# Performance work log

Measured on AMD Instinct MI355X. Metric: run time of the kernel, lower is better.

## Reference

```python
import jax, jax.numpy as jnp
import numpy as np

B, D, H = 65536, 3, 256  # collocation batch, coord dim, hidden width


def setup_inputs() -> dict:
    key = jax.random.key(0)
    ks = jax.random.split(key, 8)

    def init(k, shape, fan_in):
        return jax.random.normal(k, shape, dtype=jnp.float32) * np.float32(1.0 / np.sqrt(fan_in))

    return {
        "x": jax.random.uniform(ks[0], (B, D), dtype=jnp.float32, minval=0.1, maxval=1.0),
        "W0": init(ks[1], (D, H), D), "b0": jnp.zeros((H,), jnp.float32),
        "W1": init(ks[2], (H, H), H), "b1": jnp.zeros((H,), jnp.float32),
        "W2": init(ks[3], (H, H), H), "b2": jnp.zeros((H,), jnp.float32),
        "W3": init(ks[4], (H, H), H), "b3": jnp.zeros((H,), jnp.float32),
        "Wout": init(ks[5], (H, 1), H), "bout": jnp.zeros((1,), jnp.float32),
    }


def reference(x, W0, b0, W1, b1, W2, b2, W3, b3, Wout, bout):
    # Scalar PINN network u(xi), xi: [D]
    def u_fn(xi):
        h = jnp.tanh(xi @ W0 + b0)
        h = jnp.tanh(h @ W1 + b1)
        h = jnp.tanh(h @ W2 + b2)
        h = jnp.tanh(h @ W3 + b3)
        return (h @ Wout + bout)[0]

    u = jax.vmap(u_fn)(x)                               # [B]
    # batch_gradient: du/dx_i for every coordinate axis (Cartesian: no adjustment)
    grads = jax.vmap(jax.grad(u_fn))(x)                 # [B, D]
    # batch_hessian diagonal: d^2u/dx_i^2 via forward-over-reverse
    hess_fn = jax.jacfwd(jax.grad(u_fn))                # [D, D] per sample
    hess_diag = jax.vmap(lambda xi: jnp.diagonal(hess_fn(xi)))(x)  # [B, D]
    # pack (u, grad, hessian-diagonal) as the PDE-residual ingredients
    return jnp.concatenate([u[:, None], grads, hess_diag], axis=1)  # [B, 1+D+D]
```

## Files before the change

kernel.cpp:

```cpp
#include <hip/hip_runtime.h>
#include <hip/hip_fp16.h>

#define HDIM 256
#define MS 16
#define PAD 8
#define LDAK (HDIM + PAD)

typedef _Float16 half8 __attribute__((ext_vector_type(8)));
typedef _Float16 half4 __attribute__((ext_vector_type(4)));
typedef float f32x4 __attribute__((ext_vector_type(4)));

__device__ __forceinline__ float fast_tanh(float x) {
    float e = __expf(2.0f * x);
    return 1.0f - 2.0f * __builtin_amdgcn_rcpf(e + 1.0f);
}

__global__ __launch_bounds__(256) void pack_weights(const float* __restrict__ W1,
                                                    const float* __restrict__ W2,
                                                    const float* __restrict__ W3,
                                                    _Float16* __restrict__ out) {
    int tid = blockIdx.x * blockDim.x + threadIdx.x;
    int l = tid >> 16;
    int idx = tid & 65535;
    int k = idx >> 8;
    int n = idx & 255;
    const float* W = (l == 0) ? W1 : (l == 1) ? W2 : W3;
    out[l * 65536 + (((k >> 3) << 8) + n) * 8 + (k & 7)] = (_Float16)W[idx];
}

__global__ __launch_bounds__(256, 2)
void pinn_fused(const float* __restrict__ x,
                const float* __restrict__ W0,
                const float* __restrict__ b0,
                const float* __restrict__ b1,
                const float* __restrict__ b2,
                const float* __restrict__ b3,
                const float* __restrict__ Wout,
                const float* __restrict__ bout,
                const _Float16* __restrict__ Wp,
                float* __restrict__ out) {
    __shared__ __align__(16) _Float16 Abuf[7 * MS][LDAK];
    __shared__ float xs[MS * 3];

    const int tid  = threadIdx.x;
    const int lane = tid & 63;
    const int wid  = tid >> 6;
    const int qd   = lane >> 4;
    const int n15  = lane & 15;
    const int base = blockIdx.x * MS;

    if (tid < MS * 3) xs[tid] = x[base * 3 + tid];
    __syncthreads();

    {
        const int m = tid & 15;
        const int n0base = (tid >> 4) * 16;
        const float x0 = xs[m * 3 + 0], x1 = xs[m * 3 + 1], x2 = xs[m * 3 + 2];
        #pragma unroll
        for (int ch = 0; ch < 4; ++ch) {
            const int n0 = n0base + ch * 4;
            f32x4 w0 = *(const f32x4*)(W0 + 0 * HDIM + n0);
            f32x4 w1 = *(const f32x4*)(W0 + 1 * HDIM + n0);
            f32x4 w2 = *(const f32x4*)(W0 + 2 * HDIM + n0);
            f32x4 bv = *(const f32x4*)(b0 + n0);
            half4 h[7];
            #pragma unroll
            for (int r = 0; r < 4; ++r) {
                float z  = x0 * w0[r] + x1 * w1[r] + x2 * w2[r] + bv[r];
                float tv = fast_tanh(z);
                float dd = 1.f - tv * tv;
                float c2 = -2.f * tv * dd;
                h[0][r] = (_Float16)tv;
                h[1][r] = (_Float16)(dd * w0[r]);
                h[2][r] = (_Float16)(dd * w1[r]);
                h[3][r] = (_Float16)(dd * w2[r]);
                h[4][r] = (_Float16)(c2 * w0[r] * w0[r]);
                h[5][r] = (_Float16)(c2 * w1[r] * w1[r]);
                h[6][r] = (_Float16)(c2 * w2[r] * w2[r]);
            }
            #pragma unroll
            for (int c = 0; c < 7; ++c)
                *(half4*)&Abuf[c * MS + m][n0] = h[c];
        }
    }
    __syncthreads();

    #pragma unroll
    for (int l = 0; l < 3; ++l) {
        const _Float16* W = Wp + l * 65536;
        const float* bb = (l == 0) ? b1 : (l == 1) ? b2 : b3;

        f32x4 acc[7][4];
        #pragma unroll
        for (int c = 0; c < 7; ++c)
            #pragma unroll
            for (int t = 0; t < 4; ++t) acc[c][t] = (f32x4){0.f, 0.f, 0.f, 0.f};

        #pragma unroll
        for (int s = 0; s < 8; ++s) {
            half8 wf[4];
            #pragma unroll
            for (int t = 0; t < 4; ++t) {
                const int n = wid * 64 + t * 16 + n15;
                wf[t] = *(const half8*)(W + ((s * 4 + qd) * 256 + n) * 8);
            }
            #pragma unroll
            for (int c = 0; c < 7; ++c) {
                half8 af = *(const half8*)&Abuf[c * MS + n15][s * 32 + qd * 8];
                #pragma unroll
                for (int t = 0; t < 4; ++t)
                    acc[c][t] = __builtin_amdgcn_mfma_f32_16x16x32_f16(wf[t], af, acc[c][t], 0, 0, 0);
            }
        }
        __syncthreads();

        #pragma unroll
        for (int t = 0; t < 4; ++t) {
            const int ncol = wid * 64 + t * 16 + qd * 4;
            f32x4 bv = *(const f32x4*)(bb + ncol);
            half4 h[7];
            #pragma unroll
            for (int r = 0; r < 4; ++r) {
                float zv = acc[0][t][r] + bv[r];
                float tv = fast_tanh(zv);
                float dd = 1.f - tv * tv;
                float c2 = -2.f * tv * dd;
                h[0][r] = (_Float16)tv;
                #pragma unroll
                for (int i = 0; i < 3; ++i) {
                    float zg = acc[1 + i][t][r];
                    float zs = acc[4 + i][t][r];
                    h[1 + i][r] = (_Float16)(dd * zg);
                    h[4 + i][r] = (_Float16)(dd * zs + c2 * zg * zg);
                }
            }
            #pragma unroll
            for (int c = 0; c < 7; ++c)
                *(half4*)&Abuf[c * MS + n15][ncol] = h[c];
        }
        __syncthreads();
    }

    if (tid < 7 * MS * 2) {
        const int row = tid >> 1;
        const int h   = tid & 1;
        const _Float16* rp = &Abuf[row][h * 128];
        const float* wp = Wout + h * 128;
        float accv = 0.f;
        #pragma unroll 4
        for (int k = 0; k < 128; k += 8) {
            half8 av = *(const half8*)&rp[k];
            #pragma unroll
            for (int j = 0; j < 8; ++j) accv += (float)av[j] * wp[k + j];
        }
        accv += __shfl_xor(accv, 1, 64);
        if (h == 0) {
            const int c = row >> 4;
            const int m = row & 15;
            if (c == 0) accv += bout[0];
            out[(base + m) * 7 + c] = accv;
        }
    }
}

extern "C" void kernel_launch(void* const* d_in, const int* in_sizes, int n_in,
                              void* d_out, int out_size, void* d_ws, size_t ws_size,
                              hipStream_t stream) {
    const float* xp   = (const float*)d_in[0];
    const float* W0   = (const float*)d_in[1];
    const float* b0   = (const float*)d_in[2];
    const float* W1   = (const float*)d_in[3];
    const float* b1   = (const float*)d_in[4];
    const float* W2   = (const float*)d_in[5];
    const float* b2   = (const float*)d_in[6];
    const float* W3   = (const float*)d_in[7];
    const float* b3   = (const float*)d_in[8];
    const float* Wout = (const float*)d_in[9];
    const float* bout = (const float*)d_in[10];
    _Float16* Wp = (_Float16*)d_ws;

    pack_weights<<<768, 256, 0, stream>>>(W1, W2, W3, Wp);
    pinn_fused<<<65536 / MS, 256, 0, stream>>>(xp, W0, b0, b1, b2, b3, Wout, bout, Wp,
                                               (float*)d_out);
}
```

Baseline: 267.8 us.

## Use 512-thread blocks with XOR-swizzled LDS and vectorized weight packing

```diff
diff --git a/kernel.cpp b/kernel.cpp
--- a/kernel.cpp
+++ b/kernel.cpp
@@ -3,8 +3,6 @@
 
 #define HDIM 256
 #define MS 16
-#define PAD 8
-#define LDAK (HDIM + PAD)
 
 typedef _Float16 half8 __attribute__((ext_vector_type(8)));
 typedef _Float16 half4 __attribute__((ext_vector_type(4)));
@@ -15,20 +13,27 @@
     return 1.0f - 2.0f * __builtin_amdgcn_rcpf(e + 1.0f);
 }
 
+__device__ __forceinline__ int swz(int row, int col) {
+    return (col & 0xC7) | (((((col >> 3) ^ row)) & 7) << 3);
+}
+
 __global__ __launch_bounds__(256) void pack_weights(const float* __restrict__ W1,
                                                     const float* __restrict__ W2,
                                                     const float* __restrict__ W3,
                                                     _Float16* __restrict__ out) {
-    int tid = blockIdx.x * blockDim.x + threadIdx.x;
-    int l = tid >> 16;
-    int idx = tid & 65535;
-    int k = idx >> 8;
+    int tid = blockIdx.x * 256 + threadIdx.x;
+    int l = tid >> 13;
+    int idx = tid & 8191;
+    int kg = idx >> 8;
     int n = idx & 255;
     const float* W = (l == 0) ? W1 : (l == 1) ? W2 : W3;
-    out[l * 65536 + (((k >> 3) << 8) + n) * 8 + (k & 7)] = (_Float16)W[idx];
+    half8 v;
+    #pragma unroll
+    for (int j = 0; j < 8; ++j) v[j] = (_Float16)W[(kg * 8 + j) * 256 + n];
+    *(half8*)(out + l * 65536 + (kg * 256 + n) * 8) = v;
 }
 
-__global__ __launch_bounds__(256, 2)
+__global__ __launch_bounds__(512, 4)
 void pinn_fused(const float* __restrict__ x,
                 const float* __restrict__ W0,
                 const float* __restrict__ b0,
@@ -39,7 +44,7 @@
                 const float* __restrict__ bout,
                 const _Float16* __restrict__ Wp,
                 float* __restrict__ out) {
-    __shared__ __align__(16) _Float16 Abuf[7 * MS][LDAK];
+    __shared__ __align__(16) _Float16 Abuf[7 * MS * HDIM];
     __shared__ float xs[MS * 3];
 
     const int tid  = threadIdx.x;
@@ -53,34 +58,30 @@
     __syncthreads();
 
     {
-        const int m = tid & 15;
-        const int n0base = (tid >> 4) * 16;
+        const int m  = tid & 15;
+        const int n0 = (tid >> 4) * 8;
         const float x0 = xs[m * 3 + 0], x1 = xs[m * 3 + 1], x2 = xs[m * 3 + 2];
+        half8 h[7];
         #pragma unroll
-        for (int ch = 0; ch < 4; ++ch) {
-            const int n0 = n0base + ch * 4;
-            f32x4 w0 = *(const f32x4*)(W0 + 0 * HDIM + n0);
-            f32x4 w1 = *(const f32x4*)(W0 + 1 * HDIM + n0);
-            f32x4 w2 = *(const f32x4*)(W0 + 2 * HDIM + n0);
-            f32x4 bv = *(const f32x4*)(b0 + n0);
-            half4 h[7];
-            #pragma unroll
-            for (int r = 0; r < 4; ++r) {
-                float z  = x0 * w0[r] + x1 * w1[r] + x2 * w2[r] + bv[r];
-                float tv = fast_tanh(z);
-                float dd = 1.f - tv * tv;
-                float c2 = -2.f * tv * dd;
-                h[0][r] = (_Float16)tv;
-                h[1][r] = (_Float16)(dd * w0[r]);
-                h[2][r] = (_Float16)(dd * w1[r]);
-                h[3][r] = (_Float16)(dd * w2[r]);
-                h[4][r] = (_Float16)(c2 * w0[r] * w0[r]);
-                h[5][r] = (_Float16)(c2 * w1[r] * w1[r]);
-                h[6][r] = (_Float16)(c2 * w2[r] * w2[r]);
-            }
-            #pragma unroll
-            for (int c = 0; c < 7; ++c)
-                *(half4*)&Abuf[c * MS + m][n0] = h[c];
+        for (int r = 0; r < 8; ++r) {
+            const int n = n0 + r;
+            const float w0 = W0[n], w1 = W0[HDIM + n], w2 = W0[2 * HDIM + n];
+            float z  = x0 * w0 + x1 * w1 + x2 * w2 + b0[n];
+            float tv = fast_tanh(z);
+            float dd = 1.f - tv * tv;
+            float c2 = -2.f * tv * dd;
+            h[0][r] = (_Float16)tv;
+            h[1][r] = (_Float16)(dd * w0);
+            h[2][r] = (_Float16)(dd * w1);
+            h[3][r] = (_Float16)(dd * w2);
+            h[4][r] = (_Float16)(c2 * w0 * w0);
+            h[5][r] = (_Float16)(c2 * w1 * w1);
+            h[6][r] = (_Float16)(c2 * w2 * w2);
+        }
+        #pragma unroll
+        for (int c = 0; c < 7; ++c) {
+            const int row = c * MS + m;
+            *(half8*)&Abuf[row * HDIM + swz(row, n0)] = h[c];
         }
     }
     __syncthreads();
@@ -90,33 +91,34 @@
         const _Float16* W = Wp + l * 65536;
         const float* bb = (l == 0) ? b1 : (l == 1) ? b2 : b3;
 
-        f32x4 acc[7][4];
+        f32x4 acc[7][2];
         #pragma unroll
         for (int c = 0; c < 7; ++c)
             #pragma unroll
-            for (int t = 0; t < 4; ++t) acc[c][t] = (f32x4){0.f, 0.f, 0.f, 0.f};
+            for (int t = 0; t < 2; ++t) acc[c][t] = (f32x4){0.f, 0.f, 0.f, 0.f};
 
         #pragma unroll
         for (int s = 0; s < 8; ++s) {
-            half8 wf[4];
+            half8 wf[2];
             #pragma unroll
-            for (int t = 0; t < 4; ++t) {
-                const int n = wid * 64 + t * 16 + n15;
+            for (int t = 0; t < 2; ++t) {
+                const int n = wid * 32 + t * 16 + n15;
                 wf[t] = *(const half8*)(W + ((s * 4 + qd) * 256 + n) * 8);
             }
             #pragma unroll
             for (int c = 0; c < 7; ++c) {
-                half8 af = *(const half8*)&Abuf[c * MS + n15][s * 32 + qd * 8];
+                const int row = c * MS + n15;
+                half8 af = *(const half8*)&Abuf[row * HDIM + swz(row, s * 32 + qd * 8)];
                 #pragma unroll
-                for (int t = 0; t < 4; ++t)
+                for (int t = 0; t < 2; ++t)
                     acc[c][t] = __builtin_amdgcn_mfma_f32_16x16x32_f16(wf[t], af, acc[c][t], 0, 0, 0);
             }
         }
         __syncthreads();
 
         #pragma unroll
-        for (int t = 0; t < 4; ++t) {
-            const int ncol = wid * 64 + t * 16 + qd * 4;
+        for (int t = 0; t < 2; ++t) {
+            const int ncol = wid * 32 + t * 16 + qd * 4;
             f32x4 bv = *(const f32x4*)(bb + ncol);
             half4 h[7];
             #pragma unroll
@@ -135,25 +137,31 @@
                 }
             }
             #pragma unroll
-            for (int c = 0; c < 7; ++c)
-                *(half4*)&Abuf[c * MS + n15][ncol] = h[c];
+            for (int c = 0; c < 7; ++c) {
+                const int row = c * MS + n15;
+                *(half4*)&Abuf[row * HDIM + swz(row, ncol)] = h[c];
+            }
         }
         __syncthreads();
     }
 
-    if (tid < 7 * MS * 2) {
-        const int row = tid >> 1;
-        const int h   = tid & 1;
-        const _Float16* rp = &Abuf[row][h * 128];
-        const float* wp = Wout + h * 128;
+    if (tid < 7 * MS * 4) {
+        const int row = tid >> 2;
+        const int h   = tid & 3;
         float accv = 0.f;
-        #pragma unroll 4
-        for (int k = 0; k < 128; k += 8) {
-            half8 av = *(const half8*)&rp[k];
+        #pragma unroll
+        for (int kg = 0; kg < 8; ++kg) {
+            const int col = h * 64 + kg * 8;
+            half8 av = *(const half8*)&Abuf[row * HDIM + swz(row, col)];
+            f32x4 wa = *(const f32x4*)(Wout + col);
+            f32x4 wb = *(const f32x4*)(Wout + col + 4);
             #pragma unroll
-            for (int j = 0; j < 8; ++j) accv += (float)av[j] * wp[k + j];
+            for (int j = 0; j < 4; ++j) accv += (float)av[j] * wa[j];
+            #pragma unroll
+            for (int j = 0; j < 4; ++j) accv += (float)av[4 + j] * wb[j];
         }
         accv += __shfl_xor(accv, 1, 64);
+        accv += __shfl_xor(accv, 2, 64);
         if (h == 0) {
             const int c = row >> 4;
             const int m = row & 15;
@@ -179,7 +187,7 @@
     const float* bout = (const float*)d_in[10];
     _Float16* Wp = (_Float16*)d_ws;
 
-    pack_weights<<<768, 256, 0, stream>>>(W1, W2, W3, Wp);
-    pinn_fused<<<65536 / MS, 256, 0, stream>>>(xp, W0, b0, b1, b2, b3, Wout, bout, Wp,
+    pack_weights<<<96, 256, 0, stream>>>(W1, W2, W3, Wp);
+    pinn_fused<<<65536 / MS, 512, 0, stream>>>(xp, W0, b0, b1, b2, b3, Wout, bout, Wp,
                                                (float*)d_out);
 }
```

Result: slower. 279.6 us (+4.4%).

## Double-buffer weight and activation fragments across K-steps and layers

Applied to the files above, without the earlier changes.

```diff
diff --git a/kernel.cpp b/kernel.cpp
--- a/kernel.cpp
+++ b/kernel.cpp
@@ -3,8 +3,7 @@
 
 #define HDIM 256
 #define MS 16
-#define PAD 8
-#define LDAK (HDIM + PAD)
+#define LDAK 264
 
 typedef _Float16 half8 __attribute__((ext_vector_type(8)));
 typedef _Float16 half4 __attribute__((ext_vector_type(4)));
@@ -19,13 +18,16 @@
                                                     const float* __restrict__ W2,
                                                     const float* __restrict__ W3,
                                                     _Float16* __restrict__ out) {
-    int tid = blockIdx.x * blockDim.x + threadIdx.x;
-    int l = tid >> 16;
-    int idx = tid & 65535;
-    int k = idx >> 8;
+    int tid = blockIdx.x * 256 + threadIdx.x;
+    int l = tid >> 13;
+    int idx = tid & 8191;
+    int kg = idx >> 8;
     int n = idx & 255;
     const float* W = (l == 0) ? W1 : (l == 1) ? W2 : W3;
-    out[l * 65536 + (((k >> 3) << 8) + n) * 8 + (k & 7)] = (_Float16)W[idx];
+    half8 v;
+    #pragma unroll
+    for (int j = 0; j < 8; ++j) v[j] = (_Float16)W[(kg * 8 + j) * 256 + n];
+    *(half8*)(out + l * 65536 + (kg * 256 + n) * 8) = v;
 }
 
 __global__ __launch_bounds__(256, 2)
@@ -53,41 +55,49 @@
     __syncthreads();
 
     {
-        const int m = tid & 15;
-        const int n0base = (tid >> 4) * 16;
+        const int m  = tid & 15;
+        const int nb = (tid >> 4) * 16;
         const float x0 = xs[m * 3 + 0], x1 = xs[m * 3 + 1], x2 = xs[m * 3 + 2];
         #pragma unroll
-        for (int ch = 0; ch < 4; ++ch) {
-            const int n0 = n0base + ch * 4;
-            f32x4 w0 = *(const f32x4*)(W0 + 0 * HDIM + n0);
-            f32x4 w1 = *(const f32x4*)(W0 + 1 * HDIM + n0);
-            f32x4 w2 = *(const f32x4*)(W0 + 2 * HDIM + n0);
-            f32x4 bv = *(const f32x4*)(b0 + n0);
-            half4 h[7];
-            #pragma unroll
-            for (int r = 0; r < 4; ++r) {
-                float z  = x0 * w0[r] + x1 * w1[r] + x2 * w2[r] + bv[r];
+        for (int ch = 0; ch < 2; ++ch) {
+            const int n0 = nb + ch * 8;
+            half8 h[7];
+            #pragma unroll
+            for (int r = 0; r < 8; ++r) {
+                const int n = n0 + r;
+                const float w0 = W0[n], w1 = W0[HDIM + n], w2 = W0[2 * HDIM + n];
+                float z  = x0 * w0 + x1 * w1 + x2 * w2 + b0[n];
                 float tv = fast_tanh(z);
                 float dd = 1.f - tv * tv;
                 float c2 = -2.f * tv * dd;
                 h[0][r] = (_Float16)tv;
-                h[1][r] = (_Float16)(dd * w0[r]);
-                h[2][r] = (_Float16)(dd * w1[r]);
-                h[3][r] = (_Float16)(dd * w2[r]);
-                h[4][r] = (_Float16)(c2 * w0[r] * w0[r]);
-                h[5][r] = (_Float16)(c2 * w1[r] * w1[r]);
-                h[6][r] = (_Float16)(c2 * w2[r] * w2[r]);
+                h[1][r] = (_Float16)(dd * w0);
+                h[2][r] = (_Float16)(dd * w1);
+                h[3][r] = (_Float16)(dd * w2);
+                h[4][r] = (_Float16)(c2 * w0 * w0);
+                h[5][r] = (_Float16)(c2 * w1 * w1);
+                h[6][r] = (_Float16)(c2 * w2 * w2);
             }
             #pragma unroll
             for (int c = 0; c < 7; ++c)
-                *(half4*)&Abuf[c * MS + m][n0] = h[c];
+                *(half8*)&Abuf[c * MS + m][n0] = h[c];
         }
     }
     __syncthreads();
+
+    half8 wf[2][4];
+    {
+        #pragma unroll
+        for (int t = 0; t < 4; ++t) {
+            const int n = wid * 64 + t * 16 + n15;
+            wf[0][t] = *(const half8*)(Wp + (qd * 256 + n) * 8);
+        }
+    }
 
     #pragma unroll
     for (int l = 0; l < 3; ++l) {
-        const _Float16* W = Wp + l * 65536;
+        const _Float16* W  = Wp + l * 65536;
+        const _Float16* Wn = Wp + (l < 2 ? l + 1 : 2) * 65536;
         const float* bb = (l == 0) ? b1 : (l == 1) ? b2 : b3;
 
         f32x4 acc[7][4];
@@ -96,21 +106,35 @@
             #pragma unroll
             for (int t = 0; t < 4; ++t) acc[c][t] = (f32x4){0.f, 0.f, 0.f, 0.f};
 
+        half8 af[2][7];
+        #pragma unroll
+        for (int c = 0; c < 7; ++c)
+            af[0][c] = *(const half8*)&Abuf[c * MS + n15][qd * 8];
+
         #pragma unroll
         for (int s = 0; s < 8; ++s) {
-            half8 wf[4];
-            #pragma unroll
-            for (int t = 0; t < 4; ++t) {
-                const int n = wid * 64 + t * 16 + n15;
-                wf[t] = *(const half8*)(W + ((s * 4 + qd) * 256 + n) * 8);
+            const int cur = s & 1, nxt = cur ^ 1;
+            if (s < 7) {
+                #pragma unroll
+                for (int t = 0; t < 4; ++t) {
+                    const int n = wid * 64 + t * 16 + n15;
+                    wf[nxt][t] = *(const half8*)(W + (((s + 1) * 4 + qd) * 256 + n) * 8);
+                }
+                #pragma unroll
+                for (int c = 0; c < 7; ++c)
+                    af[nxt][c] = *(const half8*)&Abuf[c * MS + n15][(s + 1) * 32 + qd * 8];
+            } else {
+                #pragma unroll
+                for (int t = 0; t < 4; ++t) {
+                    const int n = wid * 64 + t * 16 + n15;
+                    wf[nxt][t] = *(const half8*)(Wn + (qd * 256 + n) * 8);
+                }
             }
             #pragma unroll
-            for (int c = 0; c < 7; ++c) {
-                half8 af = *(const half8*)&Abuf[c * MS + n15][s * 32 + qd * 8];
+            for (int c = 0; c < 7; ++c)
                 #pragma unroll
                 for (int t = 0; t < 4; ++t)
-                    acc[c][t] = __builtin_amdgcn_mfma_f32_16x16x32_f16(wf[t], af, acc[c][t], 0, 0, 0);
-            }
+                    acc[c][t] = __builtin_amdgcn_mfma_f32_16x16x32_f16(wf[cur][t], af[cur][c], acc[c][t], 0, 0, 0);
         }
         __syncthreads();
 
@@ -179,7 +203,7 @@
     const float* bout = (const float*)d_in[10];
     _Float16* Wp = (_Float16*)d_ws;
 
-    pack_weights<<<768, 256, 0, stream>>>(W1, W2, W3, Wp);
+    pack_weights<<<96, 256, 0, stream>>>(W1, W2, W3, Wp);
     pinn_fused<<<65536 / MS, 256, 0, stream>>>(xp, W0, b0, b1, b2, b3, Wout, bout, Wp,
                                                (float*)d_out);
 }
```

Measured after the change: 262.6 us. Within noise of the previous version (-2.0%).
